# Kernel optimization log

Measured on AMD Instinct MI355X. Metric: run time of the kernel, lower is better.

Reference implementation:

```python
import jax, jax.numpy as jnp
import numpy as np

B, DIM, L = 4, 1024, 4096
N_CODES, CODE_DIM, H = 512, 256, 8
D = DIM // H  # head_dim = 128


def setup_inputs() -> dict:
    key = jax.random.key(0)
    k1, k2, k3, k4 = jax.random.split(key, 4)
    return {
        "x": jax.random.normal(k1, (B, DIM, L), dtype=jnp.float32),
        "codes": jax.random.normal(k2, (N_CODES, CODE_DIM), dtype=jnp.float32),
        "Wk": jax.random.normal(k3, (CODE_DIM, H, D), dtype=jnp.float32) * (CODE_DIM ** -0.5),
        "Wv": jax.random.normal(k4, (CODE_DIM, H, D), dtype=jnp.float32) * (CODE_DIM ** -0.5),
    }


def reference(x, codes, Wk, Wv):
    b, xdim, l = x.shape
    h, d = Wk.shape[1], Wk.shape[2]
    scale = d ** -0.5
    # b (h d) l -> b h l d
    q = scale * jnp.transpose(x.reshape(b, h, d, l), (0, 1, 3, 2))
    k = jnp.einsum('nc,chd->hnd', codes, Wk)  # [H, N, D]
    v = jnp.einsum('nc,chd->hnd', codes, Wv)  # [H, N, D]
    logits = jnp.einsum('bhld,hmd->bhlm', q, k)  # [B, H, L, N]
    idx = jnp.argmax(logits, axis=-1)  # [B, H, L] int
    # hard one-hot attention == direct gather from v
    h_ix = jnp.arange(h)[None, :, None]  # broadcast over B, L
    out = v[h_ix, idx]  # [B, H, L, D]
    out = jnp.transpose(out, (0, 1, 3, 2)).reshape(b, h * d, l)  # b (h d) l
    return out, idx
```

## Files before the change

kernel.cpp:

```cpp
#include <hip/hip_runtime.h>
#include <cstdint>

#define L_ 4096
#define NC_ 512
#define CD_ 256
#define H_ 8
#define D_ 128
#define B_ 4
#define SCALE 0.08838834764831845f
#define TAU 3.0e-3f

typedef _Float16 f16x8 __attribute__((ext_vector_type(8)));
typedef _Float16 f16x4 __attribute__((ext_vector_type(4)));
typedef float f32x16 __attribute__((ext_vector_type(16)));
typedef float f32x4 __attribute__((ext_vector_type(4)));

__global__ __launch_bounds__(256) void kv_pre(
    const float* __restrict__ codes, const float* __restrict__ Wk,
    const float* __restrict__ Wv, _Float16* __restrict__ K16f,
    float* __restrict__ K32, float* __restrict__ V)
{
    __shared__ float clds[8][256];
    const int t = threadIdx.x, h = blockIdx.y, n0 = blockIdx.x * 8;
    {
        const float4* cs = (const float4*)(codes + (size_t)n0 * CD_);
        float4* cd = (float4*)&clds[0][0];
        cd[t] = cs[t]; cd[t + 256] = cs[t + 256];
    }
    __syncthreads();
    const int nl = t >> 5, dq = t & 31, d0 = dq * 4, n = n0 + nl;
    float ak0=0,ak1=0,ak2=0,ak3=0, av0=0,av1=0,av2=0,av3=0;
    const float4* wk4 = (const float4*)Wk;
    const float4* wv4 = (const float4*)Wv;
    for (int c = 0; c < CD_; c += 4) {
        float4 cv = *(const float4*)&clds[nl][c];
        #pragma unroll
        for (int u = 0; u < 4; ++u) {
            float cu = (u==0)?cv.x:(u==1)?cv.y:(u==2)?cv.z:cv.w;
            float4 wk = wk4[((size_t)(c+u)*H_ + h)*32 + dq];
            float4 wv = wv4[((size_t)(c+u)*H_ + h)*32 + dq];
            ak0 = fmaf(cu, wk.x, ak0); ak1 = fmaf(cu, wk.y, ak1);
            ak2 = fmaf(cu, wk.z, ak2); ak3 = fmaf(cu, wk.w, ak3);
            av0 = fmaf(cu, wv.x, av0); av1 = fmaf(cu, wv.y, av1);
            av2 = fmaf(cu, wv.z, av2); av3 = fmaf(cu, wv.w, av3);
        }
    }
    const size_t r32 = ((size_t)(h*NC_ + n))*D_ + d0;
    float4 sk; sk.x=ak0; sk.y=ak1; sk.z=ak2; sk.w=ak3;
    float4 sv; sv.x=av0; sv.y=av1; sv.z=av2; sv.w=av3;
    *(float4*)(K32 + r32) = sk;
    *(float4*)(V   + r32) = sv;
    f16x4 hk; hk[0]=(_Float16)ak0; hk[1]=(_Float16)ak1; hk[2]=(_Float16)ak2; hk[3]=(_Float16)ak3;
    const size_t a16 = ((size_t)((h*16 + (n>>5))*8 + (d0>>4))*64
                        + ((n&31) + ((d0>>3)&1)*32))*8 + (d0&7);
    *(f16x4*)(K16f + a16) = hk;
}

#define GLD_LDS16(GP, LP)                                                      \
  __builtin_amdgcn_global_load_lds(                                            \
      (const __attribute__((address_space(1))) void*)(GP),                     \
      (__attribute__((address_space(3))) void*)(LP), 16, 0, 0)

#define WAIT_VM0    asm volatile("s_waitcnt vmcnt(0)" ::: "memory")
#define WAIT_LGKM   asm volatile("s_waitcnt lgkmcnt(0)" ::: "memory")

#define QSTAGE(RD, QS)                                                         \
  _Pragma("unroll")                                                            \
  for (int i_ = 0; i_ < 4; ++i_) {                                             \
    const float* sp_ = xb + (size_t)((RD)*32 + i_*8 + (lane>>3))*L_            \
                          + l0w + (lane&7)*4;                                  \
    GLD_LDS16(sp_, (char*)(QS) + i_*1024);                                     \
  }

#define QREAD(RD, QS)                                                          \
  _Pragma("unroll")                                                            \
  for (int p_ = 0; p_ < 2; ++p_) {                                             \
    f16x8 tmp_;                                                                \
    _Pragma("unroll")                                                          \
    for (int j_ = 0; j_ < 8; ++j_)                                             \
      tmp_[j_] = (_Float16)(SCALE * (QS)[(p_*16 + hi*8 + j_)*32 + colL]);      \
    qf[(RD)*2 + p_] = tmp_;                                                    \
  }

__global__ __launch_bounds__(256, 4) void attn_main(
    const float* __restrict__ x, const _Float16* __restrict__ K16f,
    const float* __restrict__ K32, const float* __restrict__ V,
    float* __restrict__ out, float* __restrict__ idxf)
{
    __shared__ __align__(16) char smem[32768 + 2048];
    _Float16* kbuf0 = (_Float16*)smem;
    _Float16* kbuf1 = (_Float16*)(smem + 8192);
    float*    qbuf  = (float*)(smem + 32768);

    const int t = threadIdx.x;
    const int wid = t >> 6, lane = t & 63;
    const int bid = blockIdx.x;
    const int h  = bid & 7;
    const int rr_ = bid >> 3;
    const int lx = rr_ & 31, b = rr_ >> 5;
    const int l0w = lx * 128 + wid * 32;

    const float* xb = x + ((size_t)(b*1024 + h*128)) * L_;
    const int colL = lane & 31;
    const int hi = lane >> 5;
    const int laneN4 = hi * 4;

    float* qs0 = (float*)(smem + wid * 8192);
    float* qs1 = (float*)(smem + wid * 8192 + 4096);
    f16x8 qf[8];
    QSTAGE(0, qs0)
    QSTAGE(1, qs1)
    WAIT_VM0;
    QREAD(0, qs0)
    QREAD(1, qs1)
    WAIT_LGKM;
    QSTAGE(2, qs0)
    QSTAGE(3, qs1)
    WAIT_VM0;
    QREAD(2, qs0)
    QREAD(3, qs1)
    __syncthreads();

    const _Float16* kh = K16f + ((size_t)h << 16);

    GLD_LDS16(kh + (size_t)(wid*64 + lane)*8,       kbuf0 + (size_t)(wid*64)*8);
    GLD_LDS16(kh + (size_t)(256 + wid*64 + lane)*8, kbuf0 + (size_t)(256 + wid*64)*8);

    float v1 = -INFINITY, v2 = -INFINITY, v3 = -INFINITY;
    int i1 = 0, i2 = 0;

    __syncthreads();

    for (int nt = 0; nt < 16; ++nt) {
        _Float16* kcur = (nt & 1) ? kbuf1 : kbuf0;
        _Float16* knxt = (nt & 1) ? kbuf0 : kbuf1;
        if (nt < 15) {
            const _Float16* src = kh + (size_t)(nt+1)*4096;
            GLD_LDS16(src + (size_t)(wid*64 + lane)*8,       knxt + (size_t)(wid*64)*8);
            GLD_LDS16(src + (size_t)(256 + wid*64 + lane)*8, knxt + (size_t)(256 + wid*64)*8);
        }
        f32x16 acc;
        #pragma unroll
        for (int r = 0; r < 16; ++r) acc[r] = 0.f;
        #pragma unroll
        for (int ds = 0; ds < 8; ++ds) {
            f16x8 kf = *(const f16x8*)(kcur + (size_t)(ds*64 + lane)*8);
            acc = __builtin_amdgcn_mfma_f32_32x32x16_f16(kf, qf[ds], acc, 0, 0, 0);
        }
        const int nb = nt*32 + laneN4;
        #pragma unroll
        for (int r = 0; r < 16; ++r) {
            const int n = nb + (r & 3) + ((r >> 2) << 3);
            float v = acc[r];
            bool gt1 = v > v1;
            bool gt2 = v > v2;
            i2 = gt1 ? i1 : (gt2 ? n : i2);
            i1 = gt1 ? n  : i1;
            v3 = fmaxf(v3, fminf(v2, v));
            v2 = fmaxf(v2, fminf(v1, v));
            v1 = fmaxf(v1, v);
        }
        __syncthreads();
    }

    float ov1 = __shfl_xor(v1, 32), ov2 = __shfl_xor(v2, 32), ov3 = __shfl_xor(v3, 32);
    int oi1 = __shfl_xor(i1, 32), oi2 = __shfl_xor(i2, 32);
    bool sw = (ov1 > v1) || (ov1 == v1 && oi1 < i1);
    float a1 = sw ? ov1 : v1;  int ai1 = sw ? oi1 : i1;
    float b1 = sw ? v1 : ov1;  int bi1 = sw ? i1 : oi1;
    float a2 = sw ? ov2 : v2;  int ai2 = sw ? oi2 : i2;
    float b2 = sw ? v2 : ov2;
    float a3 = sw ? ov3 : v3;
    bool sec = (b1 > a2) || (b1 == a2 && bi1 < ai2);
    const float V1 = a1;             const int I1 = ai1;
    const float V2 = sec ? b1 : a2;  const int I2 = sec ? bi1 : ai2;
    const float V3 = sec ? fmaxf(a2, b2) : fmaxf(a3, b1);
    int idx = I1;

    const bool cheap = (V1 - V2 < TAU) && (V1 - V3 >= TAU);
    const bool full  = (V1 - V3 < TAU);

    unsigned long long mc = __ballot(cheap) & 0xffffffffull;
    while (mc) {
        int src = (int)__builtin_ctzll(mc); mc &= mc - 1;
        int rl = l0w + src;
        int ra = __shfl(I1, src);
        int rb = __shfl(I2, src);
        int n = hi ? rb : ra;
        f32x4 kk = *(const f32x4*)(K32 + ((size_t)(h*NC_ + n))*D_ + colL*4);
        int dd = colL * 4;
        float q0 = SCALE * xb[(size_t)(dd+0)*L_ + rl];
        float q1 = SCALE * xb[(size_t)(dd+1)*L_ + rl];
        float q2 = SCALE * xb[(size_t)(dd+2)*L_ + rl];
        float q3 = SCALE * xb[(size_t)(dd+3)*L_ + rl];
        float p = q0 * kk[0];
        p = fmaf(q1, kk[1], p); p = fmaf(q2, kk[2], p); p = fmaf(q3, kk[3], p);
        #pragma unroll
        for (int m = 1; m < 32; m <<= 1) p += __shfl_xor(p, m);
        float va = __shfl(p, 0);
        float vb = __shfl(p, 32);
        bool takeB = (vb > va) || (vb == va && rb < ra);
        int win = takeB ? rb : ra;
        if (lane == src) idx = win;
    }

    unsigned long long mf2 = __ballot(full) & 0xffffffffull;
    float* qb = qbuf + wid * 128;
    while (mf2) {
        int src = (int)__builtin_ctzll(mf2); mf2 &= mf2 - 1;
        int rl = l0w + src;
        qb[lane]      = SCALE * xb[(size_t)lane*L_ + rl];
        qb[lane + 64] = SCALE * xb[(size_t)(lane+64)*L_ + rl];
        __builtin_amdgcn_wave_barrier();
        WAIT_LGKM;
        float accs[8];
        #pragma unroll
        for (int u = 0; u < 8; ++u) accs[u] = 0.f;
        const float* kr = K32 + ((size_t)(h*NC_ + lane))*D_;
        for (int d4 = 0; d4 < 32; ++d4) {
            float qd0 = qb[d4*4+0], qd1 = qb[d4*4+1], qd2 = qb[d4*4+2], qd3 = qb[d4*4+3];
            #pragma unroll
            for (int u = 0; u < 8; ++u) {
                f32x4 kk = *(const f32x4*)(kr + (size_t)u*64*D_ + d4*4);
                accs[u] = fmaf(qd0, kk[0], accs[u]);
                accs[u] = fmaf(qd1, kk[1], accs[u]);
                accs[u] = fmaf(qd2, kk[2], accs[u]);
                accs[u] = fmaf(qd3, kk[3], accs[u]);
            }
        }
        float bv = -INFINITY; int bn = 0;
        #pragma unroll
        for (int u = 0; u < 8; ++u) {
            if (accs[u] > bv) { bv = accs[u]; bn = lane + (u << 6); }
        }
        #pragma unroll
        for (int m = 1; m < 64; m <<= 1) {
            float ov = __shfl_xor(bv, m);
            int on = __shfl_xor(bn, m);
            if (ov > bv || (ov == bv && on < bn)) { bv = ov; bn = on; }
        }
        if (lane == src) idx = bn;
        __builtin_amdgcn_wave_barrier();
    }
    idx = __shfl(idx, colL);

    const int myl = l0w + colL;
    if (!hi) idxf[((size_t)(b*H_ + h))*L_ + myl] = (float)idx;
    const f32x4* vrow = (const f32x4*)(V + ((size_t)(h*NC_ + idx))*D_);
    float* ob = out + ((size_t)(b*1024 + h*128 + hi*64))*L_ + myl;
    #pragma unroll
    for (int p = 0; p < 16; ++p) {
        f32x4 vv = vrow[hi*16 + p];
        ob[(size_t)(p*4+0)*L_] = vv[0];
        ob[(size_t)(p*4+1)*L_] = vv[1];
        ob[(size_t)(p*4+2)*L_] = vv[2];
        ob[(size_t)(p*4+3)*L_] = vv[3];
    }
}

extern "C" void kernel_launch(void* const* d_in, const int* in_sizes, int n_in,
                              void* d_out, int out_size, void* d_ws, size_t ws_size,
                              hipStream_t stream)
{
    const float* x     = (const float*)d_in[0];
    const float* codes = (const float*)d_in[1];
    const float* Wk    = (const float*)d_in[2];
    const float* Wv    = (const float*)d_in[3];

    float* out  = (float*)d_out;
    float* idxf = out + (size_t)B_ * H_ * D_ * L_;

    _Float16* K16f = (_Float16*)d_ws;
    float*    K32  = (float*)((char*)d_ws + (1u << 20));
    float*    Vf   = (float*)((char*)d_ws + (3u << 20));

    kv_pre<<<dim3(64, 8), 256, 0, stream>>>(codes, Wk, Wv, K16f, K32, Vf);
    attn_main<<<dim3(1024), 256, 0, stream>>>(x, K16f, K32, Vf, out, idxf);
}
```

Baseline: 91.77 us.

## Coalesce fp32 refinement K reads and remap kv_pre grid to 1D

The fp32 fallback path that recomputes full argmax for rows flagged as ambiguous now has each half-wave handle one code. Each lane holds four q elements and reads contiguous float4 chunks of a K row, followed by a 32-lane shuffle reduction per code. The old path had each lane stride through eight separate K rows. The kv_pre grid is also flattened to 1D with head in the low bits, so adjacent blocks share codes rows. The new refinement adds many shuffles per code (5 per code across 256 iterations), which could cost more than the memory coalescing saves. It only runs for the rare refined rows.

```diff
diff --git a/kernel.cpp b/kernel.cpp
--- a/kernel.cpp
+++ b/kernel.cpp
@@ -21,7 +21,9 @@
     float* __restrict__ K32, float* __restrict__ V)
 {
     __shared__ float clds[8][256];
-    const int t = threadIdx.x, h = blockIdx.y, n0 = blockIdx.x * 8;
+    const int t = threadIdx.x;
+    const int h  = blockIdx.x & 7;
+    const int n0 = (blockIdx.x >> 3) * 8;
     {
         const float4* cs = (const float4*)(codes + (size_t)n0 * CD_);
         float4* cd = (float4*)&clds[0][0];
@@ -213,30 +215,24 @@
         qb[lane + 64] = SCALE * xb[(size_t)(lane+64)*L_ + rl];
         __builtin_amdgcn_wave_barrier();
         WAIT_LGKM;
-        float accs[8];
-        #pragma unroll
-        for (int u = 0; u < 8; ++u) accs[u] = 0.f;
-        const float* kr = K32 + ((size_t)(h*NC_ + lane))*D_;
-        for (int d4 = 0; d4 < 32; ++d4) {
-            float qd0 = qb[d4*4+0], qd1 = qb[d4*4+1], qd2 = qb[d4*4+2], qd3 = qb[d4*4+3];
+        float q0 = qb[colL*4+0], q1 = qb[colL*4+1], q2 = qb[colL*4+2], q3 = qb[colL*4+3];
+        const f32x4* krow = (const f32x4*)(K32 + (size_t)h*NC_*D_);
+        float bv = -INFINITY; int bn = 0;
+        for (int i = 0; i < 256; i += 4) {
             #pragma unroll
-            for (int u = 0; u < 8; ++u) {
-                f32x4 kk = *(const f32x4*)(kr + (size_t)u*64*D_ + d4*4);
-                accs[u] = fmaf(qd0, kk[0], accs[u]);
-                accs[u] = fmaf(qd1, kk[1], accs[u]);
-                accs[u] = fmaf(qd2, kk[2], accs[u]);
-                accs[u] = fmaf(qd3, kk[3], accs[u]);
+            for (int u = 0; u < 4; ++u) {
+                f32x4 kk = krow[(size_t)(i+u)*64 + lane];
+                float p = q0 * kk[0];
+                p = fmaf(q1, kk[1], p); p = fmaf(q2, kk[2], p); p = fmaf(q3, kk[3], p);
+                #pragma unroll
+                for (int m = 1; m < 32; m <<= 1) p += __shfl_xor(p, m);
+                const int n = 2*(i+u) + hi;
+                if (p > bv) { bv = p; bn = n; }
             }
         }
-        float bv = -INFINITY; int bn = 0;
-        #pragma unroll
-        for (int u = 0; u < 8; ++u) {
-            if (accs[u] > bv) { bv = accs[u]; bn = lane + (u << 6); }
-        }
-        #pragma unroll
-        for (int m = 1; m < 64; m <<= 1) {
-            float ov = __shfl_xor(bv, m);
-            int on = __shfl_xor(bn, m);
+        {
+            float ov = __shfl_xor(bv, 32);
+            int on = __shfl_xor(bn, 32);
             if (ov > bv || (ov == bv && on < bn)) { bv = ov; bn = on; }
         }
         if (lane == src) idx = bn;
@@ -274,6 +270,6 @@
     float*    K32  = (float*)((char*)d_ws + (1u << 20));
     float*    Vf   = (float*)((char*)d_ws + (3u << 20));
 
-    kv_pre<<<dim3(64, 8), 256, 0, stream>>>(codes, Wk, Wv, K16f, K32, Vf);
+    kv_pre<<<dim3(512), 256, 0, stream>>>(codes, Wk, Wv, K16f, K32, Vf);
     attn_main<<<dim3(1024), 256, 0, stream>>>(x, K16f, K32, Vf, out, idxf);
 }
```

Measured after the change: 180.0 us. 1.96x slower.
